# Optimization experiments

Measured on AMD Instinct MI355X. Metric: run time of the kernel, lower is better.

## Reference

```python
import jax, jax.numpy as jnp
import numpy as np

D_MODEL = 1024
N_HEAD = 16
HEAD_DIM = D_MODEL // N_HEAD
N_POS = 4096
K_PROJ = 256  # self.k is hardcoded to 256 in the module
BATCH = 4


def setup_inputs() -> dict:
    key = jax.random.key(0)
    ks = jax.random.split(key, 11)
    s = 1.0 / np.sqrt(D_MODEL)
    return {
        "x": jax.random.normal(ks[0], (BATCH, N_POS, D_MODEL), jnp.float32),
        "Wq": jax.random.normal(ks[1], (D_MODEL, D_MODEL), jnp.float32) * s,
        "bq": jnp.zeros((D_MODEL,), jnp.float32),
        "Wk": jax.random.normal(ks[2], (D_MODEL, D_MODEL), jnp.float32) * s,
        "bk": jnp.zeros((D_MODEL,), jnp.float32),
        "Wv": jax.random.normal(ks[3], (D_MODEL, D_MODEL), jnp.float32) * s,
        "bv": jnp.zeros((D_MODEL,), jnp.float32),
        "E": jax.random.normal(ks[4], (K_PROJ, N_POS), jnp.float32),
        "F": jax.random.normal(ks[5], (K_PROJ, N_POS), jnp.float32),
        "Wo": jax.random.normal(ks[6], (D_MODEL, D_MODEL), jnp.float32) * s,
        "bo": jnp.zeros((D_MODEL,), jnp.float32),
    }


def reference(x, Wq, bq, Wk, bk, Wv, bv, E, F, Wo, bo):
    B, N, D = x.shape
    scale = jnp.sqrt(jnp.asarray(HEAD_DIM, x.dtype))
    # Q/K/V projections (nn.Linear applies x @ W.T + b)
    def proj(W, b):
        y = jnp.einsum('bnd,ed->bne', x, W) + b
        return y.reshape(B, N, N_HEAD, HEAD_DIM).transpose(0, 2, 1, 3)  # bhnd
    Q = proj(Wq, bq)
    K = proj(Wk, bk)
    V = proj(Wv, bv)
    # Linformer low-rank projections along sequence dim
    Kp = jnp.einsum('kn,bhnd->bhkd', E, K)
    Vp = jnp.einsum('kn,bhnd->bhkd', F, V)
    attn_score = jnp.einsum('bhnd,bhkd->bhnk', Q, Kp) / scale
    attn = jax.nn.softmax(attn_score, axis=-1)  # dropout is identity (drop_prob=0)
    out = jnp.einsum('bhnk,bhkd->bhnd', attn, Vp)
    out = out.transpose(0, 2, 1, 3).reshape(B, N, D)
    out = jnp.einsum('bnd,ed->bne', out, Wo) + bo
    return out, attn_score
```

## Files before the change

### kernel.cpp

```cpp
#include <hip/hip_runtime.h>

typedef _Float16 f16;
typedef __attribute__((ext_vector_type(8))) _Float16 f16x8;
typedef __attribute__((ext_vector_type(4))) _Float16 f16x4;
typedef __attribute__((ext_vector_type(4))) float f32x4;

typedef const __attribute__((address_space(1))) unsigned int* gas_ptr;
typedef __attribute__((address_space(3))) unsigned int* las_ptr;

__device__ __forceinline__ void gload16(const f16* g, f16* l) {
  __builtin_amdgcn_global_load_lds((gas_ptr)g, (las_ptr)l, 16, 0, 0);
}

#define BARRIER_LGKM() do { \
    asm volatile("s_waitcnt lgkmcnt(0)" ::: "memory"); \
    __builtin_amdgcn_sched_barrier(0); \
    __builtin_amdgcn_s_barrier(); } while (0)

template<int WM, int WN, bool OUT32>
__device__ __forceinline__ void gemm_core(
    const f16* __restrict__ A, int lda,
    const f16* __restrict__ B, int ldb,
    int kLen,
    f16* lsA, f16* lsB,
    float* __restrict__ C32, f16* __restrict__ C16, int ldc,
    float scale, const float* __restrict__ biasC, const float* __restrict__ biasR)
{
  constexpr int T   = WM * WN * 64;
  constexpr int nA  = (WM * 64 * 8) / T;
  constexpr int nB  = (WN * 64 * 8) / T;
  constexpr int RPI = T / 8;
  const int t    = threadIdx.x;
  const int lane = t & 63;
  const int wave = t >> 6;
  const int wm   = wave / WN;
  const int wn   = wave % WN;

  f32x4 acc[4][4];
  const f32x4 z4 = {0.f, 0.f, 0.f, 0.f};
#pragma unroll
  for (int i = 0; i < 4; ++i)
#pragma unroll
    for (int j = 0; j < 4; ++j) acc[i][j] = z4;

  const int r_ = t >> 3;
  const int c_ = (t & 7) * 8;
  const int ldsOff = (wave << 9);

  for (int kt = 0; kt < kLen; kt += 64) {
#pragma unroll
    for (int i = 0; i < nA; ++i) {
      const f16* g = A + (size_t)(i * RPI + r_) * lda + kt + c_;
      gload16(g, lsA + i * (T * 8) + ldsOff);
    }
#pragma unroll
    for (int i = 0; i < nB; ++i) {
      const f16* g = B + (size_t)(i * RPI + r_) * ldb + kt + c_;
      gload16(g, lsB + i * (T * 8) + ldsOff);
    }
    __syncthreads();
#pragma unroll
    for (int ks = 0; ks < 2; ++ks) {
      f16x8 af[4], bf[4];
#pragma unroll
      for (int i = 0; i < 4; ++i)
        af[i] = *(const f16x8*)&lsA[(wm * 64 + i * 16 + (lane & 15)) * 64 + ks * 32 + (lane >> 4) * 8];
#pragma unroll
      for (int j = 0; j < 4; ++j)
        bf[j] = *(const f16x8*)&lsB[(wn * 64 + j * 16 + (lane & 15)) * 64 + ks * 32 + (lane >> 4) * 8];
#pragma unroll
      for (int i = 0; i < 4; ++i)
#pragma unroll
        for (int j = 0; j < 4; ++j)
          acc[i][j] = __builtin_amdgcn_mfma_f32_16x16x32_f16(af[i], bf[j], acc[i][j], 0, 0, 0);
    }
    __syncthreads();
  }

  const int lc = lane & 15;
  const int lr = (lane >> 4) * 4;
#pragma unroll
  for (int j = 0; j < 4; ++j) {
    const int col = wn * 64 + j * 16 + lc;
    const float bC = biasC ? biasC[col] : 0.f;
#pragma unroll
    for (int i = 0; i < 4; ++i) {
      const int rbase = wm * 64 + i * 16 + lr;
#pragma unroll
      for (int r = 0; r < 4; ++r) {
        const int row = rbase + r;
        float v = acc[i][j][r] * scale + bC;
        if (biasR) v += biasR[row];
        if (OUT32) C32[(size_t)row * ldc + col] = v;
        else       C16[(size_t)row * ldc + col] = (f16)v;
      }
    }
  }
}

template<bool OUT32>
__device__ __forceinline__ void gemm256_core(
    f16 (*ls)[2][8192],
    const f16* __restrict__ Ab, int lda,
    const f16* __restrict__ Bb, int ldb,
    int kLen,
    float* __restrict__ C32, f16* __restrict__ C16, int ldc,
    const float* __restrict__ biasC)
{
  const int t    = threadIdx.x;
  const int lane = t & 63;
  const int w    = t >> 6;
  const int wm   = w >> 2;
  const int wn   = w & 3;
  const int c    = lane & 15;
  const int g    = lane >> 4;
  const int ch   = c >> 1;
  const int c1   = c & 1;
  const int jsw  = (g ^ (ch & 3)) << 4;

  const int srow = ((t >> 3) << 1) + ((t >> 2) & 1);
  const int sj   = ((t & 3) ^ ((t >> 3) & 3)) * 8;
  const int NT   = kLen >> 5;

#define STAGE_A(tile) { const int kt_ = (tile) * 32; f16* d_ = &ls[(tile) & 3][0][0]; \
    gload16(Ab + (size_t)srow * lda + kt_ + sj, d_ + t * 8); \
    gload16(Ab + (size_t)(srow + 128) * lda + kt_ + sj, d_ + 4096 + t * 8); }
#define STAGE_B(tile) { const int kt_ = (tile) * 32; f16* d_ = &ls[(tile) & 3][1][0]; \
    gload16(Bb + (size_t)srow * ldb + kt_ + sj, d_ + t * 8); \
    gload16(Bb + (size_t)(srow + 128) * ldb + kt_ + sj, d_ + 4096 + t * 8); }

  STAGE_A(0); STAGE_B(0);
  STAGE_A(1); STAGE_B(1);
  asm volatile("s_waitcnt vmcnt(4)" ::: "memory");
  __builtin_amdgcn_s_barrier();

  f32x4 acc[8][4];
  const f32x4 z4 = {0.f, 0.f, 0.f, 0.f};
#pragma unroll
  for (int i = 0; i < 8; ++i)
#pragma unroll
    for (int j = 0; j < 4; ++j) acc[i][j] = z4;

  for (int tt = 0; tt < NT; ++tt) {
    const char* lA = (const char*)&ls[tt & 3][0][0];
    const char* lB = (const char*)&ls[tt & 3][1][0];
    f16x8 af[8], bf[4];
#pragma unroll
    for (int mf = 0; mf < 4; ++mf)
      af[mf] = *(const f16x8*)(lA + (size_t)(wm * 64 + mf * 8 + ch) * 128 + c1 * 64 + jsw);
#pragma unroll
    for (int nf = 0; nf < 4; ++nf)
      bf[nf] = *(const f16x8*)(lB + (size_t)(wn * 32 + nf * 8 + ch) * 128 + c1 * 64 + jsw);
    if (tt + 2 < NT) STAGE_A(tt + 2);
    __builtin_amdgcn_s_barrier();
    __builtin_amdgcn_s_setprio(1);
#pragma unroll
    for (int mf = 0; mf < 4; ++mf)
#pragma unroll
      for (int nf = 0; nf < 4; ++nf)
        acc[mf][nf] = __builtin_amdgcn_mfma_f32_16x16x32_f16(af[mf], bf[nf], acc[mf][nf], 0, 0, 0);
    __builtin_amdgcn_s_setprio(0);
#pragma unroll
    for (int mf = 4; mf < 8; ++mf)
      af[mf] = *(const f16x8*)(lA + (size_t)(wm * 64 + mf * 8 + ch) * 128 + c1 * 64 + jsw);
    if (tt + 2 < NT) {
      STAGE_B(tt + 2);
      asm volatile("s_waitcnt vmcnt(4)" ::: "memory");
    } else {
      asm volatile("s_waitcnt vmcnt(0)" ::: "memory");
    }
    __builtin_amdgcn_s_barrier();
    __builtin_amdgcn_s_setprio(1);
#pragma unroll
    for (int mf = 4; mf < 8; ++mf)
#pragma unroll
      for (int nf = 0; nf < 4; ++nf)
        acc[mf][nf] = __builtin_amdgcn_mfma_f32_16x16x32_f16(af[mf], bf[nf], acc[mf][nf], 0, 0, 0);
    __builtin_amdgcn_s_setprio(0);
  }
#undef STAGE_A
#undef STAGE_B

#pragma unroll
  for (int nf = 0; nf < 4; ++nf) {
    const int col = wn * 64 + nf * 16 + c;
    const float bC = biasC ? biasC[col] : 0.f;
#pragma unroll
    for (int mf = 0; mf < 8; ++mf) {
      const int rbase = wm * 128 + mf * 16 + g * 4;
#pragma unroll
      for (int r = 0; r < 4; ++r) {
        const float v = acc[mf][nf][r] + bC;
        if (OUT32) __builtin_nontemporal_store(v, C32 + (size_t)(rbase + r) * ldc + col);
        else       C16[(size_t)(rbase + r) * ldc + col] = (f16)v;
      }
    }
  }
}

template<bool OUT32>
__global__ __launch_bounds__(512) void k_gemm256(
    const f16* __restrict__ A, int lda,
    const f16* __restrict__ B, int ldb,
    int kLen, int nct,
    float* __restrict__ C32, f16* __restrict__ C16, int ldc,
    const float* __restrict__ biasC)
{
  __shared__ f16 ls[4][2][8192];
  const int cpx = gridDim.x >> 3;
  const int wg  = (blockIdx.x & 7) * cpx + (blockIdx.x >> 3);
  const int rt  = wg / nct, ct = wg % nct;
  gemm256_core<OUT32>(ls,
      A + (size_t)rt * 256 * lda, lda,
      B + (size_t)ct * 256 * ldb, ldb, kLen,
      OUT32 ? C32 + (size_t)rt * 256 * ldc + ct * 256 : nullptr,
      OUT32 ? nullptr : C16 + (size_t)rt * 256 * ldc + ct * 256, ldc,
      biasC ? biasC + ct * 256 : nullptr);
}

__global__ __launch_bounds__(512) void k_exfx256(const f16* __restrict__ EF,
                                                 const f16* __restrict__ XT,
                                                 float* __restrict__ part)
{
  __shared__ f16 ls[4][2][8192];
  const int cpx = gridDim.x >> 3;
  const int wg  = (blockIdx.x & 7) * cpx + (blockIdx.x >> 3);
  const int s   = wg >> 5;
  const int rem = wg & 31;
  const int b   = rem >> 3;
  const int tile = rem & 7;
  const int rt  = tile >> 2, ct = tile & 3;
  gemm256_core<true>(ls,
      EF + (size_t)rt * 256 * 4096 + s * 512, 4096,
      XT + (size_t)b * 1024 * 4096 + (size_t)ct * 256 * 4096 + s * 512, 4096,
      512,
      part + (size_t)(s * 4 + b) * 524288 + (size_t)rt * 256 * 1024 + ct * 256,
      nullptr, 1024, nullptr);
}

__global__ __launch_bounds__(256) void k_cast_xt(const float* __restrict__ x,
                                                 f16* __restrict__ Xf,
                                                 f16* __restrict__ XT)
{
  __shared__ f16 tile[64][68];
  const int b = blockIdx.z, bi = blockIdx.y, bj = blockIdx.x;
  const int r0 = threadIdx.x >> 4;
  const int c4 = (threadIdx.x & 15) * 4;
  const float* xb = x + ((size_t)b * 4096 + (size_t)bi * 64) * 1024 + bj * 64;
#pragma unroll
  for (int rr = 0; rr < 4; ++rr) {
    const int row = rr * 16 + r0;
    const float4 v = *(const float4*)(xb + (size_t)row * 1024 + c4);
    f16x4 h = {(f16)v.x, (f16)v.y, (f16)v.z, (f16)v.w};
    *(f16x4*)&tile[row][c4] = h;
    *(f16x4*)(Xf + ((size_t)b * 4096 + (size_t)bi * 64 + row) * 1024 + bj * 64 + c4) = h;
  }
  __syncthreads();
#pragma unroll
  for (int rr = 0; rr < 4; ++rr) {
    const int col = rr * 16 + r0;
    f16x4 h = {tile[c4 + 0][col], tile[c4 + 1][col], tile[c4 + 2][col], tile[c4 + 3][col]};
    *(f16x4*)(XT + ((size_t)b * 1024 + (size_t)bj * 64 + col) * 4096 + (size_t)bi * 64 + c4) = h;
  }
}

__global__ __launch_bounds__(256) void k_cast_w(
    const float* w0, const float* w1, const float* w2,
    const float* w3, const float* w4, const float* w5, f16* __restrict__ d)
{
  const size_t i = ((size_t)blockIdx.x * 256 + threadIdx.x) * 4;
  const int seg = (int)(i >> 20);
  const float* s = (seg == 0) ? w0 : (seg == 1) ? w1 : (seg == 2) ? w2
                 : (seg == 3) ? w3 : (seg == 4) ? w4 : w5;
  const float4 v = *(const float4*)(s + (i & 1048575));
  f16x4 o = {(f16)v.x, (f16)v.y, (f16)v.z, (f16)v.w};
  *(f16x4*)(d + i) = o;
}

__global__ __launch_bounds__(256) void k_rowsum(const float* __restrict__ E,
                                                const float* __restrict__ F,
                                                float* __restrict__ rs)
{
  const int r = blockIdx.x * 4 + (threadIdx.x >> 6);
  const int lane = threadIdx.x & 63;
  const float* src = (r < 256) ? (E + (size_t)r * 4096) : (F + (size_t)(r - 256) * 4096);
  float s = 0.f;
#pragma unroll
  for (int i = 0; i < 16; ++i) {
    const float4 v = *(const float4*)(src + i * 256 + lane * 4);
    s += v.x + v.y + v.z + v.w;
  }
#pragma unroll
  for (int o = 32; o; o >>= 1) s += __shfl_xor(s, o);
  if (lane == 0) rs[r] = s;
}

__global__ __launch_bounds__(256) void k_reduce2(const float* __restrict__ part,
                                                 f16* __restrict__ EXf)
{
  const size_t i = ((size_t)blockIdx.x * 256 + threadIdx.x) * 4;
  const size_t b = i >> 19;
  const size_t idx = i & 524287;
  float a0 = 0.f, a1 = 0.f, a2 = 0.f, a3 = 0.f;
#pragma unroll
  for (int s = 0; s < 8; ++s) {
    const float4 v = *(const float4*)(part + ((size_t)s * 4 + b) * 524288 + idx);
    a0 += v.x; a1 += v.y; a2 += v.z; a3 += v.w;
  }
  f16x4 o = {(f16)a0, (f16)a1, (f16)a2, (f16)a3};
  *(f16x4*)(EXf + i) = o;
}

__global__ __launch_bounds__(256) void k_kpvp(const f16* __restrict__ EXf,
                                              const f16* __restrict__ W16,
                                              float* __restrict__ p2)
{
  __shared__ f16 lsA[128 * 64];
  __shared__ f16 lsB[128 * 64];
  const int z = blockIdx.z; const int which = z & 1; const int s = z >> 1;
  const int rt = blockIdx.y, ct = blockIdx.x;
  const f16 *A, *B;
  if (which == 0) {
    const int b = rt >> 1, r0 = (rt & 1) * 128;
    A = EXf + ((size_t)b * 512 + r0) * 1024 + s * 512;
    B = W16 + 1048576 + (size_t)ct * 128 * 1024 + s * 512;
  } else {
    const int b = ct >> 1, r0 = (ct & 1) * 128;
    A = W16 + 2 * 1048576 + (size_t)rt * 128 * 1024 + s * 512;
    B = EXf + ((size_t)b * 512 + 256 + r0) * 1024 + s * 512;
  }
  float* C = p2 + (size_t)(s * 2 + which) * 1048576 + (size_t)rt * 128 * 1024 + ct * 128;
  gemm_core<2, 2, true>(A, 1024, B, 1024, 512, lsA, lsB, C, nullptr, 1024, 1.f, nullptr, nullptr);
}

__global__ __launch_bounds__(256) void k_reduce3(const float* __restrict__ p2,
                                                 f16* __restrict__ KpVp,
                                                 const float* __restrict__ rs,
                                                 const float* __restrict__ bk,
                                                 const float* __restrict__ bv)
{
  const size_t i = ((size_t)blockIdx.x * 256 + threadIdx.x) * 4;
  const int half = (int)(i >> 20);
  const size_t j = i & 1048575;
  size_t pidx; float r1[4];
  if (half == 0) {
    const int r  = (int)((j >> 10) & 255);
    const int hd = (int)(j & 1023);
    pidx = j;
    const float se = rs[r];
#pragma unroll
    for (int t = 0; t < 4; ++t) r1[t] = se * bk[hd + t];
  } else {
    const int b  = (int)(j >> 18);
    const int hd = (int)((j >> 8) & 1023);
    const int r  = (int)(j & 255);
    pidx = (size_t)hd * 1024 + (size_t)b * 256 + r;
    const float bb = bv[hd];
#pragma unroll
    for (int t = 0; t < 4; ++t) r1[t] = bb * rs[256 + r + t];
  }
  const float4 a = *(const float4*)(p2 + (size_t)(0 * 2 + half) * 1048576 + pidx);
  const float4 c = *(const float4*)(p2 + (size_t)(1 * 2 + half) * 1048576 + pidx);
  f16x4 o = {(f16)(a.x + c.x + r1[0]), (f16)(a.y + c.y + r1[1]),
             (f16)(a.z + c.z + r1[2]), (f16)(a.w + c.w + r1[3])};
  *(f16x4*)(KpVp + i) = o;
}

__global__ __launch_bounds__(256, 2) void k_attn(const f16* __restrict__ Q,
                                                 const f16* __restrict__ Kp,
                                                 const f16* __restrict__ VpT,
                                                 float* __restrict__ S,
                                                 f16* __restrict__ OP)
{
  __shared__ char smem[81920];
  f16* lsK = (f16*)smem;
  f16* lsQ = (f16*)(smem + 32768);
  f16* lsV = (f16*)(smem + 49152);

  const int rt = blockIdx.x, h = blockIdx.y, b = blockIdx.z;
  const int t = threadIdx.x, lane = t & 63, w = t >> 6;
  const int g = lane >> 4;
  const int c = lane & 15;

  const int r_ = t >> 3;
  const int cswz = ((t & 7) * 16) ^ ((r_ & 7) << 4);
  const char* Kg = (const char*)(Kp + (size_t)b * 262144 + h * 64);
  const char* Qg = (const char*)(Q + ((size_t)b * 4096 + (size_t)rt * 128) * 1024 + h * 64);
#pragma unroll
  for (int i = 0; i < 8; ++i)
    gload16((const f16*)(Kg + (size_t)(i * 32 + r_) * 2048 + cswz),
            lsK + i * 2048 + (w << 9));
#pragma unroll
  for (int i = 0; i < 4; ++i)
    gload16((const f16*)(Qg + (size_t)(i * 32 + r_) * 2048 + cswz),
            lsQ + i * 2048 + (w << 9));
  {
    const char* Vb = (const char*)(VpT + ((size_t)b * 1024 + h * 64) * 256);
    const int vrow = lane >> 5;
    const int voff = (lane & 31) * 16;
#pragma unroll
    for (int i = 0; i < 8; ++i) {
      const int row = i * 8 + w * 2 + vrow;
      const int so = voff ^ ((row & 7) << 4);
      gload16((const f16*)(Vb + (size_t)row * 512 + so),
              (f16*)((char*)lsV + i * 4096 + w * 1024));
    }
  }
  __syncthreads();

  const int swz = (lane & 7) << 4;
  f32x4 acc[16][2];
  const f32x4 z4 = {0.f, 0.f, 0.f, 0.f};
#pragma unroll
  for (int i = 0; i < 16; ++i) { acc[i][0] = z4; acc[i][1] = z4; }
#pragma unroll
  for (int ks = 0; ks < 2; ++ks) {
    const int koff = ks * 64 + g * 16;
    f16x8 bf[2];
#pragma unroll
    for (int j = 0; j < 2; ++j) {
      const int row = w * 32 + j * 16 + c;
      bf[j] = *(const f16x8*)((const char*)lsQ + row * 128 + (koff ^ swz));
    }
#pragma unroll
    for (int i = 0; i < 16; ++i) {
      const f16x8 af = *(const f16x8*)((const char*)lsK + (i * 16 + c) * 128 + (koff ^ swz));
      acc[i][0] = __builtin_amdgcn_mfma_f32_16x16x32_f16(af, bf[0], acc[i][0], 0, 0, 0);
      acc[i][1] = __builtin_amdgcn_mfma_f32_16x16x32_f16(af, bf[1], acc[i][1], 0, 0, 0);
    }
  }

  float* Sb = S + (((size_t)(b * 16 + h)) * 4096 + (size_t)rt * 128 + w * 32) * 256;
#pragma unroll
  for (int j = 0; j < 2; ++j)
#pragma unroll
    for (int i = 0; i < 16; ++i) {
      acc[i][j] *= 0.125f;
      __builtin_nontemporal_store(acc[i][j],
          (f32x4*)(Sb + (size_t)(j * 16 + c) * 256 + i * 16 + g * 4));
    }

  f16x4 pf[16][2];
#pragma unroll
  for (int j = 0; j < 2; ++j) {
    float m = acc[0][j][0];
#pragma unroll
    for (int i = 0; i < 16; ++i)
      m = fmaxf(m, fmaxf(fmaxf(acc[i][j][0], acc[i][j][1]),
                         fmaxf(acc[i][j][2], acc[i][j][3])));
    m = fmaxf(m, __shfl_xor(m, 16));
    m = fmaxf(m, __shfl_xor(m, 32));
    float s = 0.f;
#pragma unroll
    for (int i = 0; i < 16; ++i)
#pragma unroll
      for (int r2 = 0; r2 < 4; ++r2) {
        const float e = __expf(acc[i][j][r2] - m);
        acc[i][j][r2] = e;
        s += e;
      }
    s += __shfl_xor(s, 16);
    s += __shfl_xor(s, 32);
    const float inv = 1.f / s;
#pragma unroll
    for (int i = 0; i < 16; ++i) {
      f16x4 p = {(f16)(acc[i][j][0] * inv), (f16)(acc[i][j][1] * inv),
                 (f16)(acc[i][j][2] * inv), (f16)(acc[i][j][3] * inv)};
      pf[i][j] = p;
    }
  }

  char* lsPh = (char*)smem;
  f32x4 o[2][4];
#pragma unroll
  for (int i2 = 0; i2 < 2; ++i2)
#pragma unroll
    for (int jh = 0; jh < 4; ++jh) o[i2][jh] = z4;

#pragma unroll
  for (int half = 0; half < 2; ++half) {
    BARRIER_LGKM();
#pragma unroll
    for (int j = 0; j < 2; ++j) {
      const int n = w * 32 + j * 16 + c;
      char* base = lsPh + n * 256;
#pragma unroll
      for (int i8 = 0; i8 < 8; ++i8)
        *(f16x4*)(base + ((i8 * 32 + g * 8) ^ swz)) = pf[half * 8 + i8][j];
    }
    BARRIER_LGKM();
#pragma unroll
    for (int ks4 = 0; ks4 < 4; ++ks4) {
      const int koffP = ks4 * 64 + g * 16;
      const int koffV = half * 256 + koffP;
      f16x8 pa[2];
#pragma unroll
      for (int i2 = 0; i2 < 2; ++i2) {
        const int n = w * 32 + i2 * 16 + c;
        pa[i2] = *(const f16x8*)(lsPh + n * 256 + (koffP ^ swz));
      }
#pragma unroll
      for (int jh = 0; jh < 4; ++jh) {
        const f16x8 vb = *(const f16x8*)((const char*)lsV + (jh * 16 + c) * 512 + (koffV ^ swz));
        o[0][jh] = __builtin_amdgcn_mfma_f32_16x16x32_f16(pa[0], vb, o[0][jh], 0, 0, 0);
        o[1][jh] = __builtin_amdgcn_mfma_f32_16x16x32_f16(pa[1], vb, o[1][jh], 0, 0, 0);
      }
    }
  }

  f16* Ob = OP + ((size_t)b * 4096 + (size_t)rt * 128 + w * 32) * 1024 + h * 64;
#pragma unroll
  for (int jh = 0; jh < 4; ++jh) {
    const int col = jh * 16 + c;
#pragma unroll
    for (int i2 = 0; i2 < 2; ++i2) {
      const int rb = i2 * 16 + g * 4;
#pragma unroll
      for (int r2 = 0; r2 < 4; ++r2)
        Ob[(size_t)(rb + r2) * 1024 + col] = (f16)o[i2][jh][r2];
    }
  }
}

extern "C" void kernel_launch(void* const* d_in, const int* in_sizes, int n_in,
                              void* d_out, int out_size, void* d_ws, size_t ws_size,
                              hipStream_t stream) {
  const float* x  = (const float*)d_in[0];
  const float* Wq = (const float*)d_in[1];
  const float* bq = (const float*)d_in[2];
  const float* Wk = (const float*)d_in[3];
  const float* bk = (const float*)d_in[4];
  const float* Wv = (const float*)d_in[5];
  const float* bv = (const float*)d_in[6];
  const float* E  = (const float*)d_in[7];
  const float* F  = (const float*)d_in[8];
  const float* Wo = (const float*)d_in[9];
  const float* bo = (const float*)d_in[10];

  float* out = (float*)d_out;
  float* S   = out + 16777216;

  char* w = (char*)d_ws;
  f16*   Xf     = (f16*)w;
  f16*   EXf    = (f16*)w;
  float* rowsum = (float*)(w + 4 * 1048576);
  f16*   XT     = (f16*)(w + 33554432);
  f16*   OPf    = (f16*)(w + 33554432);
  f16*   Qf     = (f16*)(w + (size_t)2 * 33554432);
  float* part2  = (float*)(w + (size_t)3 * 33554432);
  f16*   W16    = (f16*)(w + (size_t)4 * 33554432);
  f16*   EF16   = W16 + (size_t)4 * 1048576;
  f16*   KpVp   = (f16*)(w + (size_t)4 * 33554432 + 12582912);
  float* partEX = S;

  k_cast_xt<<<dim3(16, 64, 4), 256, 0, stream>>>(x, Xf, XT);
  k_cast_w<<<6144, 256, 0, stream>>>(Wq, Wk, Wv, Wo, E, F, W16);

  k_gemm256<false><<<256, 512, 0, stream>>>(
      Xf, 1024, W16, 1024, 1024, 4, nullptr, Qf, 1024, bq);

  k_rowsum<<<128, 256, 0, stream>>>(E, F, rowsum);

  k_exfx256<<<256, 512, 0, stream>>>(EF16, XT, partEX);
  k_reduce2<<<2048, 256, 0, stream>>>(partEX, EXf);

  k_kpvp<<<dim3(8, 8, 4), 256, 0, stream>>>(EXf, W16, part2);
  k_reduce3<<<2048, 256, 0, stream>>>(part2, KpVp, rowsum, bk, bv);

  k_attn<<<dim3(32, 16, 4), 256, 0, stream>>>(
      Qf, KpVp, KpVp + (size_t)4 * 262144, S, OPf);

  k_gemm256<true><<<256, 512, 0, stream>>>(
      OPf, 1024, W16 + 3 * 1048576, 1024, 1024, 4, out, nullptr, 1024, bo);
}
```

Before: 606.6 us.

## Fuse rowsum into weight cast, store split-K partials in fp16, single-pass P staging

Merges the rowsum kernel into the weight-cast kernel to drop a launch. Stores the E·X split-K partials as fp16 instead of fp32, which halves partial traffic in the reduce step but risks precision loss in the 8-way sum. The attention kernel now stages the full P tile in LDS (98KB) in one pass, removing the two-half loop and its barriers. The larger shared-memory footprint and the removed min-blocks hint lower occupancy.

```diff
diff --git a/kernel.cpp b/kernel.cpp
--- a/kernel.cpp
+++ b/kernel.cpp
@@ -11,11 +11,6 @@
 __device__ __forceinline__ void gload16(const f16* g, f16* l) {
   __builtin_amdgcn_global_load_lds((gas_ptr)g, (las_ptr)l, 16, 0, 0);
 }
-
-#define BARRIER_LGKM() do { \
-    asm volatile("s_waitcnt lgkmcnt(0)" ::: "memory"); \
-    __builtin_amdgcn_sched_barrier(0); \
-    __builtin_amdgcn_s_barrier(); } while (0)
 
 template<int WM, int WN, bool OUT32>
 __device__ __forceinline__ void gemm_core(
@@ -220,7 +215,7 @@
 
 __global__ __launch_bounds__(512) void k_exfx256(const f16* __restrict__ EF,
                                                  const f16* __restrict__ XT,
-                                                 float* __restrict__ part)
+                                                 f16* __restrict__ part)
 {
   __shared__ f16 ls[4][2][8192];
   const int cpx = gridDim.x >> 3;
@@ -230,12 +225,12 @@
   const int b   = rem >> 3;
   const int tile = rem & 7;
   const int rt  = tile >> 2, ct = tile & 3;
-  gemm256_core<true>(ls,
+  gemm256_core<false>(ls,
       EF + (size_t)rt * 256 * 4096 + s * 512, 4096,
       XT + (size_t)b * 1024 * 4096 + (size_t)ct * 256 * 4096 + s * 512, 4096,
-      512,
+      512, nullptr,
       part + (size_t)(s * 4 + b) * 524288 + (size_t)rt * 256 * 1024 + ct * 256,
-      nullptr, 1024, nullptr);
+      1024, nullptr);
 }
 
 __global__ __launch_bounds__(256) void k_cast_xt(const float* __restrict__ x,
@@ -264,51 +259,52 @@
   }
 }
 
-__global__ __launch_bounds__(256) void k_cast_w(
+__global__ __launch_bounds__(256) void k_cast_w_rs(
     const float* w0, const float* w1, const float* w2,
-    const float* w3, const float* w4, const float* w5, f16* __restrict__ d)
-{
-  const size_t i = ((size_t)blockIdx.x * 256 + threadIdx.x) * 4;
-  const int seg = (int)(i >> 20);
-  const float* s = (seg == 0) ? w0 : (seg == 1) ? w1 : (seg == 2) ? w2
-                 : (seg == 3) ? w3 : (seg == 4) ? w4 : w5;
-  const float4 v = *(const float4*)(s + (i & 1048575));
-  f16x4 o = {(f16)v.x, (f16)v.y, (f16)v.z, (f16)v.w};
-  *(f16x4*)(d + i) = o;
-}
-
-__global__ __launch_bounds__(256) void k_rowsum(const float* __restrict__ E,
-                                                const float* __restrict__ F,
-                                                float* __restrict__ rs)
-{
-  const int r = blockIdx.x * 4 + (threadIdx.x >> 6);
-  const int lane = threadIdx.x & 63;
-  const float* src = (r < 256) ? (E + (size_t)r * 4096) : (F + (size_t)(r - 256) * 4096);
-  float s = 0.f;
-#pragma unroll
-  for (int i = 0; i < 16; ++i) {
-    const float4 v = *(const float4*)(src + i * 256 + lane * 4);
-    s += v.x + v.y + v.z + v.w;
-  }
-#pragma unroll
-  for (int o = 32; o; o >>= 1) s += __shfl_xor(s, o);
-  if (lane == 0) rs[r] = s;
-}
-
-__global__ __launch_bounds__(256) void k_reduce2(const float* __restrict__ part,
+    const float* w3, const float* w4, const float* w5, f16* __restrict__ d,
+    float* __restrict__ rs)
+{
+  if (blockIdx.x < 6144) {
+    const size_t i = ((size_t)blockIdx.x * 256 + threadIdx.x) * 4;
+    const int seg = (int)(i >> 20);
+    const float* s = (seg == 0) ? w0 : (seg == 1) ? w1 : (seg == 2) ? w2
+                   : (seg == 3) ? w3 : (seg == 4) ? w4 : w5;
+    const float4 v = *(const float4*)(s + (i & 1048575));
+    f16x4 o = {(f16)v.x, (f16)v.y, (f16)v.z, (f16)v.w};
+    *(f16x4*)(d + i) = o;
+  } else {
+    const int r = (blockIdx.x - 6144) * 4 + (threadIdx.x >> 6);
+    const int lane = threadIdx.x & 63;
+    const float* src = (r < 256) ? (w4 + (size_t)r * 4096) : (w5 + (size_t)(r - 256) * 4096);
+    float s = 0.f;
+#pragma unroll
+    for (int i = 0; i < 16; ++i) {
+      const float4 v = *(const float4*)(src + i * 256 + lane * 4);
+      s += v.x + v.y + v.z + v.w;
+    }
+#pragma unroll
+    for (int o = 32; o; o >>= 1) s += __shfl_xor(s, o);
+    if (lane == 0) rs[r] = s;
+  }
+}
+
+__global__ __launch_bounds__(256) void k_reduce2(const f16* __restrict__ part,
                                                  f16* __restrict__ EXf)
 {
-  const size_t i = ((size_t)blockIdx.x * 256 + threadIdx.x) * 4;
+  const size_t i = ((size_t)blockIdx.x * 256 + threadIdx.x) * 8;
   const size_t b = i >> 19;
   const size_t idx = i & 524287;
-  float a0 = 0.f, a1 = 0.f, a2 = 0.f, a3 = 0.f;
+  float a[8] = {0.f, 0.f, 0.f, 0.f, 0.f, 0.f, 0.f, 0.f};
 #pragma unroll
   for (int s = 0; s < 8; ++s) {
-    const float4 v = *(const float4*)(part + ((size_t)s * 4 + b) * 524288 + idx);
-    a0 += v.x; a1 += v.y; a2 += v.z; a3 += v.w;
-  }
-  f16x4 o = {(f16)a0, (f16)a1, (f16)a2, (f16)a3};
-  *(f16x4*)(EXf + i) = o;
+    const f16x8 v = *(const f16x8*)(part + ((size_t)s * 4 + b) * 524288 + idx);
+#pragma unroll
+    for (int j = 0; j < 8; ++j) a[j] += (float)v[j];
+  }
+  f16x8 o;
+#pragma unroll
+  for (int j = 0; j < 8; ++j) o[j] = (f16)a[j];
+  *(f16x8*)(EXf + i) = o;
 }
 
 __global__ __launch_bounds__(256) void k_kpvp(const f16* __restrict__ EXf,
@@ -366,16 +362,16 @@
   *(f16x4*)(KpVp + i) = o;
 }
 
-__global__ __launch_bounds__(256, 2) void k_attn(const f16* __restrict__ Q,
-                                                 const f16* __restrict__ Kp,
-                                                 const f16* __restrict__ VpT,
-                                                 float* __restrict__ S,
-                                                 f16* __restrict__ OP)
-{
-  __shared__ char smem[81920];
+__global__ __launch_bounds__(256) void k_attn(const f16* __restrict__ Q,
+                                              const f16* __restrict__ Kp,
+                                              const f16* __restrict__ VpT,
+                                              float* __restrict__ S,
+                                              f16* __restrict__ OP)
+{
+  __shared__ char smem[98304];
   f16* lsK = (f16*)smem;
   f16* lsQ = (f16*)(smem + 32768);
-  f16* lsV = (f16*)(smem + 49152);
+  f16* lsV = (f16*)(smem + 65536);
 
   const int rt = blockIdx.x, h = blockIdx.y, b = blockIdx.z;
   const int t = threadIdx.x, lane = t & 63, w = t >> 6;
@@ -440,7 +436,7 @@
           (f32x4*)(Sb + (size_t)(j * 16 + c) * 256 + i * 16 + g * 4));
     }
 
-  f16x4 pf[16][2];
+  float pinv[2];
 #pragma unroll
   for (int j = 0; j < 2; ++j) {
     float m = acc[0][j][0];
@@ -461,50 +457,43 @@
       }
     s += __shfl_xor(s, 16);
     s += __shfl_xor(s, 32);
-    const float inv = 1.f / s;
+    pinv[j] = 1.f / s;
+  }
+
+  __syncthreads();
+  char* lsP = (char*)smem;
+#pragma unroll
+  for (int j = 0; j < 2; ++j) {
+    const int n = w * 32 + j * 16 + c;
+    char* base = lsP + n * 512;
 #pragma unroll
     for (int i = 0; i < 16; ++i) {
-      f16x4 p = {(f16)(acc[i][j][0] * inv), (f16)(acc[i][j][1] * inv),
-                 (f16)(acc[i][j][2] * inv), (f16)(acc[i][j][3] * inv)};
-      pf[i][j] = p;
-    }
-  }
-
-  char* lsPh = (char*)smem;
+      f16x4 p = {(f16)(acc[i][j][0] * pinv[j]), (f16)(acc[i][j][1] * pinv[j]),
+                 (f16)(acc[i][j][2] * pinv[j]), (f16)(acc[i][j][3] * pinv[j])};
+      *(f16x4*)(base + ((i * 32 + g * 8) ^ swz)) = p;
+    }
+  }
+  __syncthreads();
+
   f32x4 o[2][4];
 #pragma unroll
   for (int i2 = 0; i2 < 2; ++i2)
 #pragma unroll
     for (int jh = 0; jh < 4; ++jh) o[i2][jh] = z4;
-
-#pragma unroll
-  for (int half = 0; half < 2; ++half) {
-    BARRIER_LGKM();
-#pragma unroll
-    for (int j = 0; j < 2; ++j) {
-      const int n = w * 32 + j * 16 + c;
-      char* base = lsPh + n * 256;
-#pragma unroll
-      for (int i8 = 0; i8 < 8; ++i8)
-        *(f16x4*)(base + ((i8 * 32 + g * 8) ^ swz)) = pf[half * 8 + i8][j];
-    }
-    BARRIER_LGKM();
-#pragma unroll
-    for (int ks4 = 0; ks4 < 4; ++ks4) {
-      const int koffP = ks4 * 64 + g * 16;
-      const int koffV = half * 256 + koffP;
-      f16x8 pa[2];
-#pragma unroll
-      for (int i2 = 0; i2 < 2; ++i2) {
-        const int n = w * 32 + i2 * 16 + c;
-        pa[i2] = *(const f16x8*)(lsPh + n * 256 + (koffP ^ swz));
-      }
-#pragma unroll
-      for (int jh = 0; jh < 4; ++jh) {
-        const f16x8 vb = *(const f16x8*)((const char*)lsV + (jh * 16 + c) * 512 + (koffV ^ swz));
-        o[0][jh] = __builtin_amdgcn_mfma_f32_16x16x32_f16(pa[0], vb, o[0][jh], 0, 0, 0);
-        o[1][jh] = __builtin_amdgcn_mfma_f32_16x16x32_f16(pa[1], vb, o[1][jh], 0, 0, 0);
-      }
+#pragma unroll
+  for (int ks = 0; ks < 8; ++ks) {
+    const int koff = ks * 64 + g * 16;
+    f16x8 pa[2];
+#pragma unroll
+    for (int i2 = 0; i2 < 2; ++i2) {
+      const int n = w * 32 + i2 * 16 + c;
+      pa[i2] = *(const f16x8*)(lsP + n * 512 + (koff ^ swz));
+    }
+#pragma unroll
+    for (int jh = 0; jh < 4; ++jh) {
+      const f16x8 vb = *(const f16x8*)((const char*)lsV + (jh * 16 + c) * 512 + (koff ^ swz));
+      o[0][jh] = __builtin_amdgcn_mfma_f32_16x16x32_f16(pa[0], vb, o[0][jh], 0, 0, 0);
+      o[1][jh] = __builtin_amdgcn_mfma_f32_16x16x32_f16(pa[1], vb, o[1][jh], 0, 0, 0);
     }
   }
 
@@ -543,26 +532,24 @@
   char* w = (char*)d_ws;
   f16*   Xf     = (f16*)w;
   f16*   EXf    = (f16*)w;
-  float* rowsum = (float*)(w + 4 * 1048576);
   f16*   XT     = (f16*)(w + 33554432);
   f16*   OPf    = (f16*)(w + 33554432);
   f16*   Qf     = (f16*)(w + (size_t)2 * 33554432);
+  f16*   partEX = (f16*)(w + (size_t)3 * 33554432);
   float* part2  = (float*)(w + (size_t)3 * 33554432);
   f16*   W16    = (f16*)(w + (size_t)4 * 33554432);
   f16*   EF16   = W16 + (size_t)4 * 1048576;
   f16*   KpVp   = (f16*)(w + (size_t)4 * 33554432 + 12582912);
-  float* partEX = S;
+  float* rowsum = S;
 
   k_cast_xt<<<dim3(16, 64, 4), 256, 0, stream>>>(x, Xf, XT);
-  k_cast_w<<<6144, 256, 0, stream>>>(Wq, Wk, Wv, Wo, E, F, W16);
+  k_cast_w_rs<<<6272, 256, 0, stream>>>(Wq, Wk, Wv, Wo, E, F, W16, rowsum);
 
   k_gemm256<false><<<256, 512, 0, stream>>>(
       Xf, 1024, W16, 1024, 1024, 4, nullptr, Qf, 1024, bq);
 
-  k_rowsum<<<128, 256, 0, stream>>>(E, F, rowsum);
-
   k_exfx256<<<256, 512, 0, stream>>>(EF16, XT, partEX);
-  k_reduce2<<<2048, 256, 0, stream>>>(partEX, EXf);
+  k_reduce2<<<1024, 256, 0, stream>>>(partEX, EXf);
 
   k_kpvp<<<dim3(8, 8, 4), 256, 0, stream>>>(EXf, W16, part2);
   k_reduce3<<<2048, 256, 0, stream>>>(part2, KpVp, rowsum, bk, bv);
```

New measurement: 605.8 us. About the same (-0.1%).
